# Optimization experiments

Hardware: AMD Instinct MI355X
Metric: run time of the kernel (lower is better)

The kernel has to match this reference:

```python
import jax, jax.numpy as jnp
import numpy as np
from jax import lax

L, B, N_IN, N_OUT, K = 1024, 16, 1024, 512, 5


def setup_inputs() -> dict:
    key = jax.random.key(0)
    k0, k1, k2, k3, k4 = jax.random.split(key, 5)
    val_range = (6.0 / (N_IN + N_OUT)) ** 0.5
    x = jax.random.normal(k0, (L, B, N_IN), dtype=jnp.float32)
    weight = jax.random.uniform(k1, (N_IN, N_OUT * K), dtype=jnp.float32,
                                minval=-val_range, maxval=val_range)
    bias = jax.random.normal(k2, (N_OUT * K,), dtype=jnp.float32) * 0.1
    bias_eps = jax.random.normal(k3, (N_OUT,), dtype=jnp.float32) * 0.1
    bias_final = jax.random.normal(k4, (N_OUT * 2,), dtype=jnp.float32) * 0.1
    return {"x": x, "weight": weight, "bias": bias,
            "bias_eps": bias_eps, "bias_final": bias_final}


def reference(x, weight, bias, bias_eps, bias_final):
    # x: [L, B, n_in]; unidirectional (bidir=1), real semiring, output gate, tanh
    length, batch, n_in = x.shape
    n_out = N_OUT
    u_ = (x.reshape(-1, n_in) @ weight).reshape(length, batch, n_out, K)
    b = bias.reshape(K, n_out)  # [5, n_out]: in1, in2, f1, f2, out
    forget_bias1, forget_bias2, output_bias = b[2], b[3], b[4]
    output = jax.nn.sigmoid(u_[..., 4] + output_bias)      # [L, B, n_out]
    forget1 = jax.nn.sigmoid(u_[..., 2] + forget_bias1)
    forget2 = jax.nn.sigmoid(u_[..., 3] + forget_bias2)
    u1, u2 = u_[..., 0], u_[..., 1]
    eps = jax.nn.sigmoid(bias_eps)                          # [n_out]

    def step(carry, inp):
        c1_prev, c2_prev = carry
        f1t, f2t, u1t, u2t = inp
        c1_t = c1_prev * f1t + u1t
        c2_t = c2_prev * f2t + (eps + c1_prev) * u2t
        return (c1_t, c2_t), (c1_t, c2_t)

    init = (jnp.zeros((batch, n_out), x.dtype), jnp.zeros((batch, n_out), x.dtype))
    (c1_final, c2_final), (c1s, c2s) = lax.scan(step, init, (forget1, forget2, u1, u2))

    rho = jax.nn.sigmoid(bias_final.reshape(n_out, 2)) * 2.0
    cs = c1s * rho[:, 0] + c2s * rho[:, 1]
    gcs = jnp.tanh(output * cs)                             # [L, B, n_out]
    return gcs, c1_final, c2_final
```

## Files before the change

kernel.cpp:

```cpp
#include <hip/hip_runtime.h>
#include <cstdint>

#define LSEQ 1024
#define BATCH 16
#define NIN 1024
#define NOUT 512
#define KGATE 5
#define NCOL (NOUT * KGATE)
#define MTOT (LSEQ * BATCH)
#define CHAINS (BATCH * NOUT)
#define OUT_GCS (LSEQ * BATCH * NOUT)
#define SEG 32
#define SLEN 32
#define PLANE ((size_t)MTOT * NOUT)
#define SMP ((size_t)SEG * CHAINS)

typedef _Float16 f16x8 __attribute__((ext_vector_type(8)));
typedef _Float16 f16x4 __attribute__((ext_vector_type(4)));
typedef float f32x4 __attribute__((ext_vector_type(4)));

__device__ __forceinline__ void async16(const void* g, void* l) {
    __builtin_amdgcn_global_load_lds(
        (const __attribute__((address_space(1))) void*)(uintptr_t)g,
        (__attribute__((address_space(3))) void*)(uintptr_t)l,
        16, 0, 0);
}

__device__ __forceinline__ float fsigmoid(float x) {
    return 1.0f / (1.0f + __expf(-x));
}

__global__ void convert_x_k(const float* __restrict__ x, _Float16* __restrict__ xb, int n8) {
    int i = blockIdx.x * blockDim.x + threadIdx.x;
    if (i < n8) {
        float4 a = ((const float4*)x)[2 * i];
        float4 b = ((const float4*)x)[2 * i + 1];
        f16x8 h;
        h[0] = (_Float16)a.x; h[1] = (_Float16)a.y; h[2] = (_Float16)a.z; h[3] = (_Float16)a.w;
        h[4] = (_Float16)b.x; h[5] = (_Float16)b.y; h[6] = (_Float16)b.z; h[7] = (_Float16)b.w;
        ((f16x8*)xb)[i] = h;
    }
}

__global__ __launch_bounds__(256) void transpose_w_k(const float* __restrict__ w, _Float16* __restrict__ wT) {
    __shared__ float lds[32][33];
    int t = threadIdx.x;
    int col = t & 31;
    int rowg = t >> 5;
    int n0 = blockIdx.x * 32;
    int k0 = blockIdx.y * 32;
#pragma unroll
    for (int i = 0; i < 4; i++) {
        int r = rowg + i * 8;
        lds[r][col] = w[(size_t)(k0 + r) * NCOL + n0 + col];
    }
    __syncthreads();
#pragma unroll
    for (int i = 0; i < 4; i++) {
        int r = rowg + i * 8;
        int c = n0 + r;
        int row = (c % 5) * NOUT + (c / 5);
        wT[(size_t)row * NIN + k0 + col] = (_Float16)lds[col][r];
    }
}

__global__ __launch_bounds__(256, 2) void gemm_gates_k(const _Float16* __restrict__ A,
                                                       const _Float16* __restrict__ BT,
                                                       const float* __restrict__ bias,
                                                       _Float16* __restrict__ planes) {
    __shared__ _Float16 Al[256 * 32];
    __shared__ _Float16 Bl[128 * 32];
    int t = threadIdx.x;
    int w = t >> 6, lane = t & 63;
    int m0 = blockIdx.x * 256, n0 = blockIdx.y * 128;

    f32x4 acc[8][4] = {};

    const int q = lane >> 4, r16 = lane & 15;
    const int wm = (w >> 1) * 128, wn = (w & 1) * 64;

    for (int kk = 0; kk < NIN; kk += 32) {
#pragma unroll
        for (int cc = 0; cc < 4; cc++) {
            int c = t + cc * 256;
            int r = c >> 2, sg = c & 3;
            async16(A + (size_t)(m0 + r) * NIN + kk + sg * 8, (char*)Al + c * 16);
        }
#pragma unroll
        for (int cc = 0; cc < 2; cc++) {
            int c = t + cc * 256;
            int r = c >> 2, sg = c & 3;
            async16(BT + (size_t)(n0 + r) * NIN + kk + sg * 8, (char*)Bl + c * 16);
        }
        __syncthreads();

        f16x8 af[8], bf[4];
#pragma unroll
        for (int i = 0; i < 8; i++)
            af[i] = *(const f16x8*)(Al + (wm + i * 16 + r16) * 32 + q * 8);
#pragma unroll
        for (int j = 0; j < 4; j++)
            bf[j] = *(const f16x8*)(Bl + (wn + j * 16 + r16) * 32 + q * 8);
#pragma unroll
        for (int i = 0; i < 8; i++)
#pragma unroll
            for (int j = 0; j < 4; j++)
                acc[i][j] = __builtin_amdgcn_mfma_f32_16x16x32_f16(af[i], bf[j], acc[i][j], 0, 0, 0);
        __syncthreads();
    }

    int g = n0 >> 9;
    int nb = n0 & (NOUT - 1);
    _Float16* plane = planes + (size_t)g * PLANE;
#pragma unroll
    for (int j = 0; j < 4; j++) {
        int coln = nb + wn + j * 16 + r16;
        float bv = bias[n0 + wn + j * 16 + r16];
#pragma unroll
        for (int i = 0; i < 8; i++) {
#pragma unroll
            for (int reg = 0; reg < 4; reg++) {
                int m = m0 + wm + i * 16 + q * 4 + reg;
                float v = acc[i][j][reg];
                if (g >= 2) v = fsigmoid(v + bv);
                plane[(size_t)m * NOUT + coln] = (_Float16)v;
            }
        }
    }
}

__global__ __launch_bounds__(256) void compose_k(const _Float16* __restrict__ planes,
                                                 const float* __restrict__ beps,
                                                 float* __restrict__ SM) {
    int u = blockIdx.x * 256 + threadIdx.x;
    int t = u & (CHAINS - 1);
    int s = u >> 13;
    int n = t & (NOUT - 1);
    float eps = fsigmoid(beps[n]);
    float a11 = 1.0f, a21 = 0.0f, a22 = 1.0f, b1 = 0.0f, b2 = 0.0f;
#pragma unroll 4
    for (int j = 0; j < SLEN; j++) {
        size_t e = (size_t)(s * SLEN + j) * CHAINS + t;
        float u1 = (float)planes[e];
        float u2 = (float)planes[PLANE + e];
        float f1 = (float)planes[2 * PLANE + e];
        float f2 = (float)planes[3 * PLANE + e];
        float na11 = f1 * a11;
        float na21 = fmaf(u2, a11, f2 * a21);
        float na22 = f2 * a22;
        float nb1  = fmaf(f1, b1, u1);
        float nb2  = fmaf(u2, b1, fmaf(f2, b2, eps * u2));
        a11 = na11; a21 = na21; a22 = na22; b1 = nb1; b2 = nb2;
    }
    size_t idx = (size_t)s * CHAINS + t;
    SM[idx] = a11;
    SM[SMP + idx] = a21;
    SM[2 * SMP + idx] = a22;
    SM[3 * SMP + idx] = b1;
    SM[4 * SMP + idx] = b2;
}

__global__ __launch_bounds__(256) void segscan_k(const float* __restrict__ SM,
                                                 float* __restrict__ segc,
                                                 float* __restrict__ out) {
    int t = blockIdx.x * 256 + threadIdx.x;
    float c1 = 0.0f, c2 = 0.0f;
#pragma unroll
    for (int s = 0; s < SEG; s++) {
        size_t idx = (size_t)s * CHAINS + t;
        segc[idx] = c1;
        segc[SMP + idx] = c2;
        float a11 = SM[idx];
        float a21 = SM[SMP + idx];
        float a22 = SM[2 * SMP + idx];
        float b1  = SM[3 * SMP + idx];
        float b2  = SM[4 * SMP + idx];
        float c1n = fmaf(a11, c1, b1);
        float c2n = fmaf(a21, c1, fmaf(a22, c2, b2));
        c1 = c1n; c2 = c2n;
    }
    out[OUT_GCS + t] = c1;
    out[OUT_GCS + CHAINS + t] = c2;
}

__global__ __launch_bounds__(256) void apply_k(const _Float16* __restrict__ planes,
                                               const float* __restrict__ segc,
                                               const float* __restrict__ beps,
                                               const float* __restrict__ bfin,
                                               float* __restrict__ out) {
    int u = blockIdx.x * 256 + threadIdx.x;
    int t = u & (CHAINS - 1);
    int s = u >> 13;
    int n = t & (NOUT - 1);
    float eps  = fsigmoid(beps[n]);
    float rho0 = 2.0f * fsigmoid(bfin[2 * n]);
    float rho1 = 2.0f * fsigmoid(bfin[2 * n + 1]);
    size_t idx = (size_t)s * CHAINS + t;
    float c1 = segc[idx];
    float c2 = segc[SMP + idx];
#pragma unroll 4
    for (int j = 0; j < SLEN; j++) {
        size_t e = (size_t)(s * SLEN + j) * CHAINS + t;
        float u1 = (float)planes[e];
        float u2 = (float)planes[PLANE + e];
        float f1 = (float)planes[2 * PLANE + e];
        float f2 = (float)planes[3 * PLANE + e];
        float o  = (float)planes[4 * PLANE + e];
        float c1p = c1;
        c1 = fmaf(c1p, f1, u1);
        c2 = fmaf(c2, f2, (eps + c1p) * u2);
        float cs = fmaf(c1, rho0, c2 * rho1);
        float y = o * cs;
        y = fminf(9.0f, fmaxf(-9.0f, y));
        float ex = __expf(2.0f * y);
        out[e] = (ex - 1.0f) / (ex + 1.0f);
    }
}

extern "C" void kernel_launch(void* const* d_in, const int* in_sizes, int n_in,
                              void* d_out, int out_size, void* d_ws, size_t ws_size,
                              hipStream_t stream) {
    const float* x    = (const float*)d_in[0];
    const float* wgt  = (const float*)d_in[1];
    const float* bias = (const float*)d_in[2];
    const float* beps = (const float*)d_in[3];
    const float* bfin = (const float*)d_in[4];
    float* out = (float*)d_out;

    char* p = (char*)d_ws;
    _Float16* wT     = (_Float16*)p; p += (size_t)NCOL * NIN * 2;
    _Float16* xb     = (_Float16*)p; p += (size_t)MTOT * NIN * 2;
    _Float16* planes = (_Float16*)p; p += 5 * PLANE * 2;
    float* SM        = (float*)p;    p += 5 * SMP * 4;
    float* segc      = (float*)p;    p += 2 * SMP * 4;

    transpose_w_k<<<dim3(NCOL / 32, NIN / 32), 256, 0, stream>>>(wgt, wT);

    int n8 = MTOT * NIN / 8;
    convert_x_k<<<dim3((n8 + 255) / 256), 256, 0, stream>>>(x, xb, n8);

    gemm_gates_k<<<dim3(MTOT / 256, NCOL / 128), 256, 0, stream>>>(xb, wT, bias, planes);

    compose_k<<<dim3(CHAINS * SEG / 256), 256, 0, stream>>>(planes, beps, SM);
    segscan_k<<<dim3(CHAINS / 256), 256, 0, stream>>>(SM, segc, out);
    apply_k<<<dim3(CHAINS * SEG / 256), 256, 0, stream>>>(planes, segc, beps, bfin, out);
}
```

Measured before the change: 288.8 us.

## Fuse scan stages into one decoupled-lookback kernel with register-held gates

Merges the compose, segment-scan and apply kernels into a single kernel. Each block composes its segment's affine transform, waits on a flag from the previous segment's block, then publishes its end state. The gate values are packed as pairs of halves in registers, so the planes are read from global memory once instead of twice, and two kernel launches plus the SM/segc round-trip are removed. The serial chain of flag waits across 32 segments and the higher register pressure may limit the gain. Correctness depends on blocks being scheduled in order, which is not guaranteed, so it risks deadlock.

Measured after the change: 666.6 us. 2.31x slower.

```diff
diff --git a/kernel.cpp b/kernel.cpp
--- a/kernel.cpp
+++ b/kernel.cpp
@@ -13,10 +13,9 @@
 #define SEG 32
 #define SLEN 32
 #define PLANE ((size_t)MTOT * NOUT)
-#define SMP ((size_t)SEG * CHAINS)
+#define NCG (CHAINS / 256)
 
 typedef _Float16 f16x8 __attribute__((ext_vector_type(8)));
-typedef _Float16 f16x4 __attribute__((ext_vector_type(4)));
 typedef float f32x4 __attribute__((ext_vector_type(4)));
 
 __device__ __forceinline__ void async16(const void* g, void* l) {
@@ -28,6 +27,12 @@
 
 __device__ __forceinline__ float fsigmoid(float x) {
     return 1.0f / (1.0f + __expf(-x));
+}
+
+__device__ __forceinline__ float h2f(unsigned short u) {
+    _Float16 h;
+    __builtin_memcpy(&h, &u, 2);
+    return (float)h;
 }
 
 __global__ void convert_x_k(const float* __restrict__ x, _Float16* __restrict__ xb, int n8) {
@@ -129,22 +134,46 @@
     }
 }
 
-__global__ __launch_bounds__(256) void compose_k(const _Float16* __restrict__ planes,
-                                                 const float* __restrict__ beps,
-                                                 float* __restrict__ SM) {
-    int u = blockIdx.x * 256 + threadIdx.x;
-    int t = u & (CHAINS - 1);
-    int s = u >> 13;
-    int n = t & (NOUT - 1);
+__global__ __launch_bounds__(256) void scan_fused_k(const _Float16* __restrict__ planes,
+                                                    const float* __restrict__ beps,
+                                                    const float* __restrict__ bfin,
+                                                    float* __restrict__ st,
+                                                    int* __restrict__ flags,
+                                                    float* __restrict__ out) {
+    int bid = blockIdx.x;
+    int s = bid >> 5;
+    int cg = bid & 31;
+    int tid = threadIdx.x;
+    int chain = cg * 256 + tid;
+    int n = chain & (NOUT - 1);
+    const unsigned short* gp = (const unsigned short*)planes;
+
     float eps = fsigmoid(beps[n]);
+
+    unsigned int pu1[16], pu2[16], pf1[16], pf2[16], po[16];
     float a11 = 1.0f, a21 = 0.0f, a22 = 1.0f, b1 = 0.0f, b2 = 0.0f;
-#pragma unroll 4
+#pragma unroll
     for (int j = 0; j < SLEN; j++) {
-        size_t e = (size_t)(s * SLEN + j) * CHAINS + t;
-        float u1 = (float)planes[e];
-        float u2 = (float)planes[PLANE + e];
-        float f1 = (float)planes[2 * PLANE + e];
-        float f2 = (float)planes[3 * PLANE + e];
+        size_t e = (size_t)(s * SLEN + j) * CHAINS + chain;
+        unsigned short hu1 = gp[e];
+        unsigned short hu2 = gp[PLANE + e];
+        unsigned short hf1 = gp[2 * PLANE + e];
+        unsigned short hf2 = gp[3 * PLANE + e];
+        unsigned short ho  = gp[4 * PLANE + e];
+        if (j & 1) {
+            pu1[j >> 1] |= (unsigned int)hu1 << 16;
+            pu2[j >> 1] |= (unsigned int)hu2 << 16;
+            pf1[j >> 1] |= (unsigned int)hf1 << 16;
+            pf2[j >> 1] |= (unsigned int)hf2 << 16;
+            po[j >> 1]  |= (unsigned int)ho  << 16;
+        } else {
+            pu1[j >> 1] = hu1;
+            pu2[j >> 1] = hu2;
+            pf1[j >> 1] = hf1;
+            pf2[j >> 1] = hf2;
+            po[j >> 1]  = ho;
+        }
+        float u1 = h2f(hu1), u2 = h2f(hu2), f1 = h2f(hf1), f2 = h2f(hf2);
         float na11 = f1 * a11;
         float na21 = fmaf(u2, a11, f2 * a21);
         float na22 = f2 * a22;
@@ -152,60 +181,48 @@
         float nb2  = fmaf(u2, b1, fmaf(f2, b2, eps * u2));
         a11 = na11; a21 = na21; a22 = na22; b1 = nb1; b2 = nb2;
     }
-    size_t idx = (size_t)s * CHAINS + t;
-    SM[idx] = a11;
-    SM[SMP + idx] = a21;
-    SM[2 * SMP + idx] = a22;
-    SM[3 * SMP + idx] = b1;
-    SM[4 * SMP + idx] = b2;
-}
-
-__global__ __launch_bounds__(256) void segscan_k(const float* __restrict__ SM,
-                                                 float* __restrict__ segc,
-                                                 float* __restrict__ out) {
-    int t = blockIdx.x * 256 + threadIdx.x;
-    float c1 = 0.0f, c2 = 0.0f;
-#pragma unroll
-    for (int s = 0; s < SEG; s++) {
-        size_t idx = (size_t)s * CHAINS + t;
-        segc[idx] = c1;
-        segc[SMP + idx] = c2;
-        float a11 = SM[idx];
-        float a21 = SM[SMP + idx];
-        float a22 = SM[2 * SMP + idx];
-        float b1  = SM[3 * SMP + idx];
-        float b2  = SM[4 * SMP + idx];
-        float c1n = fmaf(a11, c1, b1);
-        float c2n = fmaf(a21, c1, fmaf(a22, c2, b2));
-        c1 = c1n; c2 = c2n;
-    }
-    out[OUT_GCS + t] = c1;
-    out[OUT_GCS + CHAINS + t] = c2;
-}
-
-__global__ __launch_bounds__(256) void apply_k(const _Float16* __restrict__ planes,
-                                               const float* __restrict__ segc,
-                                               const float* __restrict__ beps,
-                                               const float* __restrict__ bfin,
-                                               float* __restrict__ out) {
-    int u = blockIdx.x * 256 + threadIdx.x;
-    int t = u & (CHAINS - 1);
-    int s = u >> 13;
-    int n = t & (NOUT - 1);
-    float eps  = fsigmoid(beps[n]);
+
+    float c1s = 0.0f, c2s = 0.0f;
+    if (s > 0) {
+        if (tid == 0) {
+            while (__hip_atomic_load(&flags[(s - 1) * NCG + cg],
+                                     __ATOMIC_ACQUIRE, __HIP_MEMORY_SCOPE_AGENT) == 0)
+                __builtin_amdgcn_s_sleep(2);
+        }
+        __syncthreads();
+        size_t pidx = (size_t)(s - 1) * 2 * CHAINS + chain;
+        c1s = __hip_atomic_load(&st[pidx], __ATOMIC_RELAXED, __HIP_MEMORY_SCOPE_AGENT);
+        c2s = __hip_atomic_load(&st[pidx + CHAINS], __ATOMIC_RELAXED, __HIP_MEMORY_SCOPE_AGENT);
+    }
+    float c1e = fmaf(a11, c1s, b1);
+    float c2e = fmaf(a21, c1s, fmaf(a22, c2s, b2));
+    if (s < SEG - 1) {
+        size_t oidx = (size_t)s * 2 * CHAINS + chain;
+        __hip_atomic_store(&st[oidx], c1e, __ATOMIC_RELAXED, __HIP_MEMORY_SCOPE_AGENT);
+        __hip_atomic_store(&st[oidx + CHAINS], c2e, __ATOMIC_RELAXED, __HIP_MEMORY_SCOPE_AGENT);
+        __syncthreads();
+        if (tid == 0) {
+            __threadfence();
+            __hip_atomic_store(&flags[s * NCG + cg], 1, __ATOMIC_RELEASE, __HIP_MEMORY_SCOPE_AGENT);
+        }
+    } else {
+        out[OUT_GCS + chain] = c1e;
+        out[OUT_GCS + CHAINS + chain] = c2e;
+    }
+
     float rho0 = 2.0f * fsigmoid(bfin[2 * n]);
     float rho1 = 2.0f * fsigmoid(bfin[2 * n + 1]);
-    size_t idx = (size_t)s * CHAINS + t;
-    float c1 = segc[idx];
-    float c2 = segc[SMP + idx];
-#pragma unroll 4
+    float c1 = c1s, c2 = c2s;
+#pragma unroll
     for (int j = 0; j < SLEN; j++) {
-        size_t e = (size_t)(s * SLEN + j) * CHAINS + t;
-        float u1 = (float)planes[e];
-        float u2 = (float)planes[PLANE + e];
-        float f1 = (float)planes[2 * PLANE + e];
-        float f2 = (float)planes[3 * PLANE + e];
-        float o  = (float)planes[4 * PLANE + e];
+        unsigned int wu1 = pu1[j >> 1], wu2 = pu2[j >> 1];
+        unsigned int wf1 = pf1[j >> 1], wf2 = pf2[j >> 1], wo = po[j >> 1];
+        int sh = (j & 1) * 16;
+        float u1 = h2f((unsigned short)(wu1 >> sh));
+        float u2 = h2f((unsigned short)(wu2 >> sh));
+        float f1 = h2f((unsigned short)(wf1 >> sh));
+        float f2 = h2f((unsigned short)(wf2 >> sh));
+        float o  = h2f((unsigned short)(wo  >> sh));
         float c1p = c1;
         c1 = fmaf(c1p, f1, u1);
         c2 = fmaf(c2, f2, (eps + c1p) * u2);
@@ -213,7 +230,7 @@
         float y = o * cs;
         y = fminf(9.0f, fmaxf(-9.0f, y));
         float ex = __expf(2.0f * y);
-        out[e] = (ex - 1.0f) / (ex + 1.0f);
+        out[(size_t)(s * SLEN + j) * CHAINS + chain] = (ex - 1.0f) / (ex + 1.0f);
     }
 }
 
@@ -231,8 +248,10 @@
     _Float16* wT     = (_Float16*)p; p += (size_t)NCOL * NIN * 2;
     _Float16* xb     = (_Float16*)p; p += (size_t)MTOT * NIN * 2;
     _Float16* planes = (_Float16*)p; p += 5 * PLANE * 2;
-    float* SM        = (float*)p;    p += 5 * SMP * 4;
-    float* segc      = (float*)p;    p += 2 * SMP * 4;
+    float* st        = (float*)p;    p += (size_t)SEG * 2 * CHAINS * 4;
+    int* flags       = (int*)p;      p += (size_t)SEG * NCG * 4;
+
+    hipMemsetAsync(flags, 0, (size_t)SEG * NCG * 4, stream);
 
     transpose_w_k<<<dim3(NCOL / 32, NIN / 32), 256, 0, stream>>>(wgt, wT);
 
@@ -241,7 +260,5 @@
 
     gemm_gates_k<<<dim3(MTOT / 256, NCOL / 128), 256, 0, stream>>>(xb, wT, bias, planes);
 
-    compose_k<<<dim3(CHAINS * SEG / 256), 256, 0, stream>>>(planes, beps, SM);
-    segscan_k<<<dim3(CHAINS / 256), 256, 0, stream>>>(SM, segc, out);
-    apply_k<<<dim3(CHAINS * SEG / 256), 256, 0, stream>>>(planes, segc, beps, bfin, out);
-}
+    scan_fused_k<<<dim3(SEG * NCG), 256, 0, stream>>>(planes, beps, bfin, st, flags, out);
+}
```
